# Kernel optimization log

Hardware: AMD Instinct MI355X
Metric: run time of the kernel (lower is better)

Reference implementation:

```python
import jax, jax.numpy as jnp
import numpy as np

B, T_ENC, T_DEC = 32, 512, 512
N_MELS, PRENET, ENC_H, ATTN_H, DEC_H, ATTN_D, N_FILT, KSIZE = 80, 256, 512, 1024, 1024, 128, 32, 31


def _lstm_cell(x, h, c, wih, whh, bih, bhh):
    gates = x @ wih.T + h @ whh.T + bih + bhh  # (B, 4H)
    i, f, g, o = jnp.split(gates, 4, axis=-1)  # torch LSTMCell gate order
    c2 = jax.nn.sigmoid(f) * c + jax.nn.sigmoid(i) * jnp.tanh(g)
    h2 = jax.nn.sigmoid(o) * jnp.tanh(c2)
    return h2, c2


def setup_inputs() -> dict:
    key = jax.random.key(0)
    ks = jax.random.split(key, 24)
    s = lambda k, shape, scale: jax.random.normal(k, shape, dtype=jnp.float32) * scale
    inp = {
        'encoder_output': s(ks[0], (B, T_ENC, ENC_H), 1.0),
        'targets': s(ks[1], (B, T_DEC, N_MELS), 1.0),
        'prenet_w1': s(ks[2], (PRENET, N_MELS), 0.05),
        'prenet_b1': jnp.zeros((PRENET,), jnp.float32),
        'prenet_w2': s(ks[3], (PRENET, PRENET), 0.05),
        'prenet_b2': jnp.zeros((PRENET,), jnp.float32),
        'M_w': s(ks[4], (ATTN_D, ENC_H), 0.04),
        'Q_w': s(ks[5], (ATTN_D, ATTN_H), 0.03),
        'W_w': s(ks[6], (1, ATTN_D), 0.08),
        'L_w': s(ks[7], (ATTN_D, N_FILT), 0.1),
        'conv_w': s(ks[8], (N_FILT, 2, KSIZE), 0.1),
        'attn_wih': s(ks[9], (4 * ATTN_H, ENC_H + PRENET), 0.02),
        'attn_whh': s(ks[10], (4 * ATTN_H, ATTN_H), 0.02),
        'attn_bih': jnp.zeros((4 * ATTN_H,), jnp.float32),
        'attn_bhh': jnp.zeros((4 * ATTN_H,), jnp.float32),
        'dec_wih': s(ks[11], (4 * DEC_H, ATTN_H + ENC_H), 0.02),
        'dec_whh': s(ks[12], (4 * DEC_H, DEC_H), 0.02),
        'dec_bih': jnp.zeros((4 * DEC_H,), jnp.float32),
        'dec_bhh': jnp.zeros((4 * DEC_H,), jnp.float32),
        'proj_w': s(ks[13], (N_MELS, DEC_H + ENC_H), 0.02),
        'proj_b': jnp.zeros((N_MELS,), jnp.float32),
    }
    return inp


def _decoder(encoder_output, targets, prenet_w1, prenet_b1, prenet_w2, prenet_b2,
             M_w, Q_w, W_w, L_w, conv_w,
             attn_wih, attn_whh, attn_bih, attn_bhh,
             dec_wih, dec_whh, dec_bih, dec_bhh, proj_w, proj_b):
    b, t_enc, _ = encoder_output.shape
    t_dec = targets.shape[1]
    pad = (KSIZE - 1) // 2

    # prenet over [zeros ; targets][:, :t_dec]  (eval mode: dropout off)
    dec_in = jnp.concatenate([jnp.zeros((b, 1, N_MELS), targets.dtype), targets], axis=1)[:, :t_dec]
    h = jax.nn.relu(dec_in @ prenet_w1.T + prenet_b1)
    prenet_out = jax.nn.relu(h @ prenet_w2.T + prenet_b2)  # (B, T_dec, prenet)

    processed_enc = encoder_output @ M_w.T  # (B, T_enc, attn_dim)

    def step(carry, x):
        ah, ac, dh, dc, aw, aws, ctx = carry
        # attention LSTM
        cell_in = jnp.concatenate([x, ctx], axis=-1)
        ah, ac = _lstm_cell(cell_in, ah, ac, attn_wih, attn_whh, attn_bih, attn_bhh)
        # location-sensitive attention
        prev_attn = jnp.stack([aw, aws], axis=1)  # (B, 2, T_enc)
        pa = jax.lax.conv_general_dilated(prev_attn, conv_w, (1,), [(pad, pad)],
                                          dimension_numbers=('NCH', 'OIH', 'NCH'))  # (B, F, T)
        pa = jnp.einsum('bft,df->btd', pa, L_w)  # (B, T, attn_dim)
        q = (ah @ Q_w.T)[:, None, :]  # (B, 1, attn_dim)
        energies = jnp.tanh(q + processed_enc + pa) @ W_w[0]  # (B, T)
        aw = jax.nn.softmax(energies, axis=1)
        ctx = jnp.einsum('bt,bte->be', aw, encoder_output)
        aws = aws + aw
        # decoder LSTM
        dcell_in = jnp.concatenate([ah, ctx], axis=-1)
        dh, dc = _lstm_cell(dcell_in, dh, dc, dec_wih, dec_whh, dec_bih, dec_bhh)
        out = jnp.concatenate([dh, ctx], axis=-1) @ proj_w.T + proj_b  # (B, n_mels)
        return (ah, ac, dh, dc, aw, aws, ctx), (out, aw)

    z = lambda d: jnp.zeros((b, d), encoder_output.dtype)
    carry0 = (z(ATTN_H), z(ATTN_H), z(DEC_H), z(DEC_H), z(t_enc), z(t_enc), z(ENC_H))
    xs = jnp.swapaxes(prenet_out, 0, 1)  # (T_dec, B, prenet)
    _, (mels, aligns) = jax.lax.scan(step, carry0, xs)
    mel_outputs = jnp.swapaxes(mels, 0, 1)      # (B, T_dec, n_mels)
    alignments = jnp.swapaxes(aligns, 0, 1)     # (B, T_dec, T_enc)
    return mel_outputs, alignments


def reference(encoder_output, targets, prenet_w1, prenet_b1, prenet_w2, prenet_b2,
              M_w, Q_w, W_w, L_w, conv_w,
              attn_wih, attn_whh, attn_bih, attn_bhh,
              dec_wih, dec_whh, dec_bih, dec_bhh, proj_w, proj_b):
    return _decoder(encoder_output, targets, prenet_w1, prenet_b1, prenet_w2, prenet_b2,
                    M_w, Q_w, W_w, L_w, conv_w,
                    attn_wih, attn_whh, attn_bih, attn_bhh,
                    dec_wih, dec_whh, dec_bih, dec_bhh, proj_w, proj_b)
```

## Files before the change

### kernel.cpp

```cpp
#include <hip/hip_runtime.h>
#include <hip/hip_fp16.h>
#include <cstddef>

typedef unsigned int uint32;

#define B_   32
#define TE_  512
#define TD_  512
#define NM_  80
#define PRE_ 256
#define EH_  512
#define AH_  1024
#define AD_  128

__device__ __forceinline__ float sigf(float x) { return 1.0f / (1.0f + expf(-x)); }

__device__ __forceinline__ float agl(const float* p) {
  return __hip_atomic_load(p, __ATOMIC_RELAXED, __HIP_MEMORY_SCOPE_AGENT);
}
__device__ __forceinline__ void ags(float* p, float v) {
  __hip_atomic_store(p, v, __ATOMIC_RELAXED, __HIP_MEMORY_SCOPE_AGENT);
}

__device__ __forceinline__ void gsync(uint32* bar, unsigned bep) {
  __syncthreads();
  if (threadIdx.x == 0) {
    asm volatile("s_waitcnt vmcnt(0)" ::: "memory");
    uint32* leaf = bar + (blockIdx.x >> 5) * 32;
    uint32* root = bar + 256;
    uint32 prev = __hip_atomic_fetch_add(leaf, 1u, __ATOMIC_RELAXED, __HIP_MEMORY_SCOPE_AGENT);
    if (prev + 1u == 32u * bep)
      __hip_atomic_fetch_add(root, 1u, __ATOMIC_RELAXED, __HIP_MEMORY_SCOPE_AGENT);
    int spins = 0;
    while (__hip_atomic_load(root, __ATOMIC_RELAXED, __HIP_MEMORY_SCOPE_AGENT) < 8u * bep) {
      __builtin_amdgcn_s_sleep(2);
      if (++spins > 20000000) break;
    }
  }
  __syncthreads();
}

__device__ __forceinline__ float rowsum16(float v) {
  int vi;
  vi = __float_as_int(v);
  v += __int_as_float(__builtin_amdgcn_update_dpp(0, vi, 0xB1, 0xF, 0xF, true));
  vi = __float_as_int(v);
  v += __int_as_float(__builtin_amdgcn_update_dpp(0, vi, 0x4E, 0xF, 0xF, true));
  vi = __float_as_int(v);
  v += __int_as_float(__builtin_amdgcn_update_dpp(0, vi, 0x124, 0xF, 0xF, true));
  vi = __float_as_int(v);
  v += __int_as_float(__builtin_amdgcn_update_dpp(0, vi, 0x128, 0xF, 0xF, true));
  return v;
}

__global__ __launch_bounds__(256) void k_pack_lstm2(
    const float* __restrict__ awih, const float* __restrict__ awhh,
    const float* __restrict__ dwih, const float* __restrict__ dwhh,
    uint32* __restrict__ wal, uint32* __restrict__ wdl, uint32* __restrict__ wdt)
{
  long gid = blockIdx.x * 256L + threadIdx.x;
  const long N1 = 3686400L, N2 = 4603904L, N3 = 655360L;
  if (gid < N1) {
    int blk = (int)(gid / 28800), rem = (int)(gid % 28800);
    int r2 = rem % 900;
    int ks = rem / 900;
    uint32 out = 0;
    if (r2 < 896) {
      int kq = r2 >> 4, rd = r2 & 15;
      int k = kq * 32 + ks;
      int rp0 = blk * 32 + 2 * rd, rp1 = rp0 + 1;
      int row0 = (rp0 & 3) * 1024 + (rp0 >> 2);
      int row1 = (rp1 & 3) * 1024 + (rp1 >> 2);
      float w0 = (k < 768) ? awih[(size_t)row0 * 768 + k] : awhh[(size_t)row0 * 1024 + k - 768];
      float w1 = (k < 768) ? awih[(size_t)row1 * 768 + k] : awhh[(size_t)row1 * 1024 + k - 768];
      __half2 h = __floats2half2_rn(w0, w1);
      out = *(uint32*)&h;
    }
    wal[gid] = out;
  } else if (gid < N1 + N2) {
    long g = gid - N1;
    int blk = (int)(g / 35968), rem = (int)(g % 35968);
    int r2 = rem % 1124;
    int ks = rem / 1124;
    uint32 out = 0;
    if (r2 < 1120) {
      int kq = r2 >> 4, rd = r2 & 15;
      int k = kq * 32 + ks;
      int rp0 = blk * 32 + 2 * rd, rp1 = rp0 + 1;
      int row0 = (rp0 & 3) * 1024 + (rp0 >> 2);
      int row1 = (rp1 & 3) * 1024 + (rp1 >> 2);
      float w0 = (k < 1536) ? dwih[(size_t)row0 * 1536 + k] : dwhh[(size_t)row0 * 1024 + k - 1536];
      float w1 = (k < 1536) ? dwih[(size_t)row1 * 1536 + k] : dwhh[(size_t)row1 * 1024 + k - 1536];
      __half2 h = __floats2half2_rn(w0, w1);
      out = *(uint32*)&h;
    }
    wdl[g] = out;
  } else if (gid < N1 + N2 + N3) {
    long g = gid - N1 - N2;
    int blk = (int)(g / 5120), rem = (int)(g % 5120);
    int rd2 = rem & 3, rg = (rem >> 2) & 3, ks = (rem >> 4) & 31, i = rem >> 9;
    int k = 2240 + 32 * i + ks;
    int r0 = rg * 8 + 2 * rd2;
    int rp0 = blk * 32 + r0, rp1 = rp0 + 1;
    int row0 = (rp0 & 3) * 1024 + (rp0 >> 2);
    int row1 = (rp1 & 3) * 1024 + (rp1 >> 2);
    float w0 = (k < 1536) ? dwih[(size_t)row0 * 1536 + k] : dwhh[(size_t)row0 * 1024 + k - 1536];
    float w1 = (k < 1536) ? dwih[(size_t)row1 * 1536 + k] : dwhh[(size_t)row1 * 1024 + k - 1536];
    __half2 h = __floats2half2_rn(w0, w1);
    wdt[g] = *(uint32*)&h;
  }
}

__global__ __launch_bounds__(256) void k_pack_small(
    const float* __restrict__ w1, const float* __restrict__ w2,
    const float* __restrict__ mw, const float* __restrict__ pw,
    const float* __restrict__ abih, const float* __restrict__ abhh,
    const float* __restrict__ dbih, const float* __restrict__ dbhh,
    const float* __restrict__ lw, const float* __restrict__ cw,
    float* __restrict__ w1t, float* __restrict__ w2t, float* __restrict__ mt,
    float* __restrict__ pjt, float* __restrict__ ba, float* __restrict__ bd,
    float* __restrict__ lc)
{
  int gid = blockIdx.x * 256 + threadIdx.x;
  if (gid < 20480) { int k = gid / 256, j = gid % 256; w1t[gid] = w1[j * 80 + k]; return; }
  gid -= 20480;
  if (gid < 65536) { int k = gid / 256, j = gid % 256; w2t[gid] = w2[j * 256 + k]; return; }
  gid -= 65536;
  if (gid < 65536) { int e = gid / 128, d = gid % 128; mt[gid] = mw[d * 512 + e]; return; }
  gid -= 65536;
  if (gid < 122880) { int k = gid / 80, m = gid % 80; pjt[gid] = pw[m * 1536 + k]; return; }
  gid -= 122880;
  if (gid < 4096) { int j = gid >> 2, g = gid & 3, row = g * 1024 + j; ba[gid] = abih[row] + abhh[row]; return; }
  gid -= 4096;
  if (gid < 4096) { int j = gid >> 2, g = gid & 3, row = g * 1024 + j; bd[gid] = dbih[row] + dbhh[row]; return; }
  gid -= 4096;
  if (gid < 7936) {
    int c = gid / (31 * 128), rem = gid % (31 * 128);
    int kk = rem / 128, d = rem % 128;
    float s = 0.f;
    for (int f = 0; f < 32; ++f) s += lw[d * 32 + f] * cw[(f * 2 + c) * 31 + kk];
    lc[gid] = s;
  }
}

__global__ __launch_bounds__(256) void k_prenet(
    const float* __restrict__ targets, const float* __restrict__ w1t,
    const float* __restrict__ b1, const float* __restrict__ w2t,
    const float* __restrict__ b2, float* __restrict__ pn)
{
  int t = blockIdx.x, tid = threadIdx.x;
  __shared__ float X[32][80];
  __shared__ float h1[256][33];
  for (int i = tid; i < 2560; i += 256) {
    int b = i / 80, m = i % 80;
    X[b][m] = (t == 0) ? 0.f : targets[((size_t)b * TD_ + (t - 1)) * NM_ + m];
  }
  __syncthreads();
  int j = tid;
  float bj = b1[j];
  for (int bt = 0; bt < 4; ++bt) {
    float acc[8];
#pragma unroll
    for (int i = 0; i < 8; ++i) acc[i] = bj;
    for (int k = 0; k < 80; ++k) {
      float w = w1t[k * 256 + j];
#pragma unroll
      for (int i = 0; i < 8; ++i) acc[i] += w * X[bt * 8 + i][k];
    }
#pragma unroll
    for (int i = 0; i < 8; ++i) h1[j][bt * 8 + i] = fmaxf(acc[i], 0.f);
  }
  __syncthreads();
  float cj = b2[j];
  float* out = pn + (size_t)t * PRE_ * B_;
  for (int bt = 0; bt < 4; ++bt) {
    float acc[8];
#pragma unroll
    for (int i = 0; i < 8; ++i) acc[i] = cj;
    for (int k = 0; k < 256; ++k) {
      float w = w2t[k * 256 + j];
#pragma unroll
      for (int i = 0; i < 8; ++i) acc[i] += w * h1[k][bt * 8 + i];
    }
#pragma unroll
    for (int i = 0; i < 8; ++i) out[j * 32 + bt * 8 + i] = fmaxf(acc[i], 0.f);
  }
}

__global__ __launch_bounds__(256) void k_penc(
    const float* __restrict__ enc, const float* __restrict__ mt,
    float* __restrict__ penc)
{
  int t = blockIdx.x, tid = threadIdx.x;
  __shared__ float encL[32][256];
  __shared__ float red[128][8][2];
  int d = tid & 127, s = tid >> 7;
  float acc[4][8];
#pragma unroll
  for (int bt = 0; bt < 4; ++bt)
#pragma unroll
    for (int i = 0; i < 8; ++i) acc[bt][i] = 0.f;
  for (int eh = 0; eh < 2; ++eh) {
    for (int i = tid; i < 8192; i += 256) {
      int b = i >> 8, e = i & 255;
      encL[b][e] = enc[((size_t)b * TE_ + t) * EH_ + eh * 256 + e];
    }
    __syncthreads();
    for (int bt = 0; bt < 4; ++bt) {
      for (int el = s * 128; el < s * 128 + 128; ++el) {
        float w = mt[(eh * 256 + el) * 128 + d];
#pragma unroll
        for (int i = 0; i < 8; ++i) acc[bt][i] += w * encL[bt * 8 + i][el];
      }
    }
    __syncthreads();
  }
  for (int bt = 0; bt < 4; ++bt) {
#pragma unroll
    for (int i = 0; i < 8; ++i) red[d][i][s] = acc[bt][i];
    __syncthreads();
    if (s == 0) {
#pragma unroll
      for (int i = 0; i < 8; ++i)
        penc[((size_t)t * AD_ + d) * 32 + bt * 8 + i] = red[d][i][0] + red[d][i][1];
    }
    __syncthreads();
  }
}

__global__ __launch_bounds__(256) void k_enct(
    const float* __restrict__ enc, __half* __restrict__ enct)
{
  int blk = blockIdx.x, tid = threadIdx.x;
  int b = blk >> 6, t0 = ((blk >> 3) & 7) * 64, e0 = (blk & 7) * 64;
  __shared__ float tile[64][65];
  for (int i = 0; i < 16; ++i) {
    int tl = i * 4 + (tid >> 6), e = tid & 63;
    tile[tl][e] = enc[((size_t)b * TE_ + t0 + tl) * EH_ + e0 + e];
  }
  __syncthreads();
  for (int i = 0; i < 16; ++i) {
    int el = i * 4 + (tid >> 6), tl = tid & 63;
    enct[((size_t)b * EH_ + e0 + el) * TE_ + t0 + tl] = __float2half(tile[tl][el]);
  }
}

struct KP {
  const uint32* wal; const uint32* wdl; const uint4* wdt;
  const float* pn; const float* penc; const __half* enct;
  const float* qw; const float* ww; const float* pjt; const float* pjb;
  const float* lc; const float* ba; const float* bd;
  float* ahv; float* ac; float* dhv; float* dc; float* ctxv;
  float* awv; float* awsv;
  float* enp; float* mel; float* align;
  uint32* bar; int pv;
};

__device__ __forceinline__ void fma2(uint4 wv, const float* __restrict__ XC,
                                     int xb, float* acc)
{
  const __half2* hp = (const __half2*)&wv;
  float w[8];
#pragma unroll
  for (int d = 0; d < 4; ++d) {
    float2 f = __half22float2(hp[d]);
    w[2 * d] = f.x; w[2 * d + 1] = f.y;
  }
  float4 xa = *(const float4*)&XC[xb];
  float4 xc2 = *(const float4*)&XC[xb + 4];
  float x[8] = {xa.x, xa.y, xa.z, xa.w, xc2.x, xc2.y, xc2.z, xc2.w};
#pragma unroll
  for (int ri = 0; ri < 8; ++ri)
#pragma unroll
    for (int bi = 0; bi < 8; ++bi)
      acc[ri * 8 + bi] = fmaf(w[ri], x[bi], acc[ri * 8 + bi]);
}

__device__ __forceinline__ void lstm_finish(
    float* acc, float* __restrict__ GT, const float* __restrict__ bias,
    float* __restrict__ cst, float* __restrict__ hout,
    int rp0, int tid, int ks, int bq, int rg)
{
#pragma unroll
  for (int i = 0; i < 64; ++i) {
    float v = rowsum16(acc[i]);
    acc[i] = v + __shfl_xor(v, 16);
  }
  if (ks == 0) {
#pragma unroll
    for (int ri = 0; ri < 8; ++ri) {
      *(float4*)&GT[(rg * 8 + ri) * 32 + bq * 8] =
          make_float4(acc[ri * 8 + 0], acc[ri * 8 + 1], acc[ri * 8 + 2], acc[ri * 8 + 3]);
      *(float4*)&GT[(rg * 8 + ri) * 32 + bq * 8 + 4] =
          make_float4(acc[ri * 8 + 4], acc[ri * 8 + 5], acc[ri * 8 + 6], acc[ri * 8 + 7]);
    }
  }
  __syncthreads();
  if (tid < 256) {
    int jl = tid >> 5, b = tid & 31;
    float gi = GT[(jl * 4 + 0) * 32 + b] + bias[rp0 + jl * 4 + 0];
    float gf = GT[(jl * 4 + 1) * 32 + b] + bias[rp0 + jl * 4 + 1];
    float gg = GT[(jl * 4 + 2) * 32 + b] + bias[rp0 + jl * 4 + 2];
    float go = GT[(jl * 4 + 3) * 32 + b] + bias[rp0 + jl * 4 + 3];
    int j = (rp0 >> 2) + jl;
    float c0 = cst[j * 32 + b];
    float c2 = sigf(gf) * c0 + sigf(gi) * tanhf(gg);
    float h2 = sigf(go) * tanhf(c2);
    cst[j * 32 + b] = c2;
    ags(&hout[j * 32 + b], h2);
  }
}

__device__ __forceinline__ void run_lstm_a(const KP& p, int t,
    const float* __restrict__ ah_in, const float* __restrict__ ctx_in,
    float* __restrict__ ah_out,
    uint32* WlU, float* XC, float* GT, int tid, int ks, int bq, int rg,
    int kidx, int b4, int blk)
{
  float acc[64];
#pragma unroll
  for (int i = 0; i < 64; ++i) acc[i] = 0.f;
  const float* xp0 = p.pn + (size_t)t * 8192;
  const int wb = ks * 900 + rg * 4;
  const int xr = ks * 36 + bq * 8;
  auto srcA = [&](int kg) -> const float* {
    return (kg < 256) ? xp0 + (size_t)kg * 32
         : (kg < 768) ? ctx_in + (size_t)(kg - 256) * 32
                      : ah_in + (size_t)(kg - 768) * 32;
  };
  float4 st0 = *(const float4*)(srcA(kidx) + b4);
  float4 st1 = *(const float4*)(srcA(64 + kidx) + b4);
  for (int cb = 0; cb < 28; cb += 2) {
    __syncthreads();
    *(float4*)&XC[kidx * 36 + b4] = st0;
    __syncthreads();
    if (cb + 2 < 28) st0 = *(const float4*)(srcA((cb + 2) * 64 + kidx) + b4);
    fma2(*(const uint4*)&WlU[wb + (2 * cb) * 16], XC, xr, acc);
    fma2(*(const uint4*)&WlU[wb + (2 * cb + 1) * 16], XC, xr + 32 * 36, acc);
    __syncthreads();
    *(float4*)&XC[kidx * 36 + b4] = st1;
    __syncthreads();
    if (cb + 3 < 28) st1 = *(const float4*)(srcA((cb + 3) * 64 + kidx) + b4);
    fma2(*(const uint4*)&WlU[wb + (2 * cb + 2) * 16], XC, xr, acc);
    fma2(*(const uint4*)&WlU[wb + (2 * cb + 3) * 16], XC, xr + 32 * 36, acc);
  }
  lstm_finish(acc, GT, p.ba, p.ac, ah_out, blk * 32, tid, ks, bq, rg);
}

__device__ __forceinline__ void run_lstm_d(const KP& p,
    const float* __restrict__ xp0, const float* __restrict__ xp1,
    const float* __restrict__ xp2, float* __restrict__ dh_w,
    uint32* WlU, float* XC, float* GT,
    int tid, int ks, int bq, int rg, int kidx, int b4, int blk)
{
  float acc[64];
#pragma unroll
  for (int i = 0; i < 64; ++i) acc[i] = 0.f;
  const int wb = ks * 1124 + rg * 4;
  const int xr = ks * 36 + bq * 8;
  auto srcD = [&](int kg) -> const float* {
    return (kg < 1024) ? xp0 + (size_t)kg * 32
         : (kg < 1536) ? xp1 + (size_t)(kg - 1024) * 32
                       : xp2 + (size_t)(kg - 1536) * 32;
  };
  float4 st0 = *(const float4*)(srcD(kidx) + b4);
  float4 st1 = *(const float4*)(srcD(64 + kidx) + b4);
  for (int cb = 0; cb < 32; cb += 2) {
    __syncthreads();
    *(float4*)&XC[kidx * 36 + b4] = st0;
    __syncthreads();
    st0 = *(const float4*)(srcD((cb + 2) * 64 + kidx) + b4);
    fma2(*(const uint4*)&WlU[wb + (2 * cb) * 16], XC, xr, acc);
    fma2(*(const uint4*)&WlU[wb + (2 * cb + 1) * 16], XC, xr + 32 * 36, acc);
    __syncthreads();
    *(float4*)&XC[kidx * 36 + b4] = st1;
    __syncthreads();
    st1 = *(const float4*)(srcD((cb + 3) * 64 + kidx) + b4);
    fma2(*(const uint4*)&WlU[wb + (2 * cb + 2) * 16], XC, xr, acc);
    fma2(*(const uint4*)&WlU[wb + (2 * cb + 3) * 16], XC, xr + 32 * 36, acc);
  }
  const uint4* wg = p.wdt + (size_t)(blk - 128) * 1280;
  const int wi = ks * 4 + rg;
  uint4 twA0, twB0, twA1, twB1;
  __syncthreads(); *(float4*)&XC[kidx * 36 + b4] = st0; __syncthreads();
  st0 = *(const float4*)(srcD(34 * 64 + kidx) + b4);
  twA0 = wg[0 * 128 + wi]; twB0 = wg[1 * 128 + wi];
  fma2(*(const uint4*)&WlU[wb + 64 * 16], XC, xr, acc);
  fma2(*(const uint4*)&WlU[wb + 65 * 16], XC, xr + 32 * 36, acc);
  __syncthreads(); *(float4*)&XC[kidx * 36 + b4] = st1; __syncthreads();
  st1 = *(const float4*)(srcD(35 * 64 + kidx) + b4);
  twA1 = wg[2 * 128 + wi]; twB1 = wg[3 * 128 + wi];
  fma2(*(const uint4*)&WlU[wb + 66 * 16], XC, xr, acc);
  fma2(*(const uint4*)&WlU[wb + 67 * 16], XC, xr + 32 * 36, acc);
  __syncthreads(); *(float4*)&XC[kidx * 36 + b4] = st0; __syncthreads();
  st0 = *(const float4*)(srcD(36 * 64 + kidx) + b4);
  fma2(*(const uint4*)&WlU[wb + 68 * 16], XC, xr, acc);
  fma2(*(const uint4*)&WlU[wb + 69 * 16], XC, xr + 32 * 36, acc);
  __syncthreads(); *(float4*)&XC[kidx * 36 + b4] = st1; __syncthreads();
  st1 = *(const float4*)(srcD(37 * 64 + kidx) + b4);
  fma2(twA0, XC, xr, acc); fma2(twB0, XC, xr + 32 * 36, acc);
  twA0 = wg[4 * 128 + wi]; twB0 = wg[5 * 128 + wi];
  __syncthreads(); *(float4*)&XC[kidx * 36 + b4] = st0; __syncthreads();
  st0 = *(const float4*)(srcD(38 * 64 + kidx) + b4);
  fma2(twA1, XC, xr, acc); fma2(twB1, XC, xr + 32 * 36, acc);
  twA1 = wg[6 * 128 + wi]; twB1 = wg[7 * 128 + wi];
  __syncthreads(); *(float4*)&XC[kidx * 36 + b4] = st1; __syncthreads();
  st1 = *(const float4*)(srcD(39 * 64 + kidx) + b4);
  fma2(twA0, XC, xr, acc); fma2(twB0, XC, xr + 32 * 36, acc);
  twA0 = wg[8 * 128 + wi]; twB0 = wg[9 * 128 + wi];
  __syncthreads(); *(float4*)&XC[kidx * 36 + b4] = st0; __syncthreads();
  fma2(twA1, XC, xr, acc); fma2(twB1, XC, xr + 32 * 36, acc);
  __syncthreads(); *(float4*)&XC[kidx * 36 + b4] = st1; __syncthreads();
  fma2(twA0, XC, xr, acc); fma2(twB0, XC, xr + 32 * 36, acc);
  lstm_finish(acc, GT, p.bd, p.dc, dh_w, (blk - 128) * 32, tid, ks, bq, rg);
}

__device__ __forceinline__ void mel_block(
    const float* __restrict__ dhp, const float* __restrict__ ctp,
    const float* __restrict__ pjt, const float* __restrict__ pjb,
    float* __restrict__ mel, int bb, int tt, float* S, int tid)
{
  float* xo = S + 1536;
  float* ro = S + 3072;
  for (int i = tid; i < 1536; i += 512)
    xo[i] = (i < 1024) ? dhp[i * 32 + bb] : ctp[(i - 1024) * 32 + bb];
  __syncthreads();
  if (tid < 480) {
    int m = tid % 80, k2 = tid / 80;
    float a2 = 0.f;
    for (int k = k2 * 256; k < k2 * 256 + 256; ++k) a2 += pjt[k * 80 + m] * xo[k];
    ro[m * 8 + k2] = a2;
  }
  __syncthreads();
  if (tid < 80) {
    float s3 = pjb[tid];
#pragma unroll
    for (int k = 0; k < 6; ++k) s3 += ro[tid * 8 + k];
    mel[((size_t)bb * TD_ + tt) * NM_ + tid] = s3;
  }
}

__global__ __launch_bounds__(512) void k_step(KP p)
{
  extern __shared__ float LDSF[];
  const int blk = blockIdx.x, tid = threadIdx.x;
  const int ks = tid & 31, bq = (tid >> 5) & 3, rg = tid >> 7;
  const int kidx = tid >> 3, b4 = (tid & 7) * 4;
  const bool isA = blk < 128;
  float* SC = LDSF + (isA ? 28800 : 35968);
  float* XC = SC;
  float* GT = SC + 2304;
  uint32* WlU = (uint32*)LDSF;
  unsigned bep = 0;

  {
    const uint32* src = isA ? p.wal + (size_t)blk * 28800
                            : p.wdl + (size_t)(blk - 128) * 35968;
    int n4 = isA ? 7200 : 8992;
    for (int i = tid; i < n4; i += 512)
      ((uint4*)WlU)[i] = ((const uint4*)src)[i];
  }
  __syncthreads();

  for (int t = 0; t < TD_; ++t) {
    const int vc = t % p.pv;
    const int vn = (t + 1) % p.pv;
    const int vp = (t > 0) ? (t - 1) % p.pv : 0;
    const float* ah_in  = p.ahv + (size_t)vc * 32768;
    float*       ah_out = p.ahv + (size_t)vn * 32768;
    const float* ctx_in = p.ctxv + (size_t)vc * 16384;
    float*       ctx_out= p.ctxv + (size_t)vn * 16384;

    if (isA) {
      run_lstm_a(p, t, ah_in, ctx_in, ah_out, WlU, XC, GT, tid, ks, bq, rg, kidx, b4, blk);
    } else if (t > 0) {
      run_lstm_d(p, ah_in, ctx_in,
                 p.dhv + (size_t)vp * 32768, p.dhv + (size_t)vc * 32768,
                 WlU, XC, GT, tid, ks, bq, rg, kidx, b4, blk);
    }
    bep += 1; gsync(p.bar, bep);
    {
      int tc = blk >> 3, ds = blk & 7;
      int t0 = tc * 16, d0 = ds * 16;
      float* qs  = SC;
      float* wws = SC + 512;
      float* AHC = SC + 528;
      float* win = SC + 528;
      float* lcs = SC + 528 + 2944;

      const float* awsrc  = p.awv  + (size_t)vc * 16384;
      const float* awssrc = p.awsv + (size_t)vc * 16384;
      float winr[6];
#pragma unroll
      for (int k = 0; k < 6; ++k) {
        int i = tid + k * 512;
        float v = 0.f;
        if (i < 2944) {
          int c = i / 1472, r = (i >> 5) % 46, bbw = i & 31;
          int tg = t0 - 15 + r;
          if (tg >= 0 && tg < 512) v = (c ? awssrc : awsrc)[tg * 32 + bbw];
        }
        winr[k] = v;
      }
      float lcr[2];
#pragma unroll
      for (int k = 0; k < 2; ++k) {
        int i = tid + k * 512;
        lcr[k] = 0.f;
        if (i < 992) {
          int c = i / 496, kk = (i >> 4) % 31, dl2 = i & 15;
          lcr[k] = p.lc[(c * 31 + kk) * 128 + d0 + dl2];
        }
      }
      const int bbE = tid & 31, thE = tid >> 5;
      const int ttE = t0 + thE;
      float pencr[16];
#pragma unroll
      for (int dl2 = 0; dl2 < 16; ++dl2)
        pencr[dl2] = p.penc[((size_t)ttE * 128 + d0 + dl2) * 32 + bbE];
      float wwr = (tid < 16) ? p.ww[d0 + tid] : 0.f;

      int bb2 = tid & 31, dl = tid >> 5;
      const float* ahsrc = p.ahv + (size_t)vn * 32768;
      const float* qbase = p.qw + (size_t)(d0 + dl) * 1024;
      float qacc = 0.f;
      float4 sq0 = *(const float4*)(ahsrc + 0 * 2048 + tid * 4);
      float4 sq1 = *(const float4*)(ahsrc + 1 * 2048 + tid * 4);
      for (int cb = 0; cb < 16; cb += 2) {
        __syncthreads();
        *(float4*)(AHC + tid * 4) = sq0;
        __syncthreads();
        if (cb + 2 < 16) sq0 = *(const float4*)(ahsrc + (cb + 2) * 2048 + tid * 4);
        {
          const float* qrow = qbase + cb * 64;
#pragma unroll
          for (int jj = 0; jj < 64; jj += 4) {
            float4 qv = *(const float4*)(qrow + jj);
            qacc = fmaf(qv.x, AHC[(jj + 0) * 32 + bb2], qacc);
            qacc = fmaf(qv.y, AHC[(jj + 1) * 32 + bb2], qacc);
            qacc = fmaf(qv.z, AHC[(jj + 2) * 32 + bb2], qacc);
            qacc = fmaf(qv.w, AHC[(jj + 3) * 32 + bb2], qacc);
          }
        }
        __syncthreads();
        *(float4*)(AHC + tid * 4) = sq1;
        __syncthreads();
        if (cb + 3 < 16) sq1 = *(const float4*)(ahsrc + (cb + 3) * 2048 + tid * 4);
        {
          const float* qrow = qbase + (cb + 1) * 64;
#pragma unroll
          for (int jj = 0; jj < 64; jj += 4) {
            float4 qv = *(const float4*)(qrow + jj);
            qacc = fmaf(qv.x, AHC[(jj + 0) * 32 + bb2], qacc);
            qacc = fmaf(qv.y, AHC[(jj + 1) * 32 + bb2], qacc);
            qacc = fmaf(qv.z, AHC[(jj + 2) * 32 + bb2], qacc);
            qacc = fmaf(qv.w, AHC[(jj + 3) * 32 + bb2], qacc);
          }
        }
      }
      __syncthreads();
      qs[dl * 32 + bb2] = qacc;
      if (tid < 16) wws[tid] = wwr;
#pragma unroll
      for (int k = 0; k < 6; ++k) { int i = tid + k * 512; if (i < 2944) win[i] = winr[k]; }
#pragma unroll
      for (int k = 0; k < 2; ++k) { int i = tid + k * 512; if (i < 992) lcs[i] = lcr[k]; }
      __syncthreads();
      {
        float pa[16];
#pragma unroll
        for (int i = 0; i < 16; ++i) pa[i] = 0.f;
        for (int c = 0; c < 2; ++c) {
          for (int kk = 0; kk < 31; ++kk) {
            float wv = win[c * 1472 + (thE + kk) * 32 + bbE];
            const float4* lr = (const float4*)(lcs + c * 496 + kk * 16);
            float4 l0 = lr[0], l1 = lr[1], l2 = lr[2], l3 = lr[3];
            pa[0]  += l0.x * wv; pa[1]  += l0.y * wv; pa[2]  += l0.z * wv; pa[3]  += l0.w * wv;
            pa[4]  += l1.x * wv; pa[5]  += l1.y * wv; pa[6]  += l1.z * wv; pa[7]  += l1.w * wv;
            pa[8]  += l2.x * wv; pa[9]  += l2.y * wv; pa[10] += l2.z * wv; pa[11] += l2.w * wv;
            pa[12] += l3.x * wv; pa[13] += l3.y * wv; pa[14] += l3.z * wv; pa[15] += l3.w * wv;
          }
        }
        float epv = 0.f;
#pragma unroll
        for (int dl2 = 0; dl2 < 16; ++dl2) {
          float v = qs[dl2 * 32 + bbE] + pencr[dl2] + pa[dl2];
          epv += wws[dl2] * tanhf(v);
        }
        ags(&p.enp[(size_t)bbE * 4096 + ttE * 8 + ds], epv);
      }
    }
    bep += 1; gsync(p.bar, bep);
    {
      int bb = blk >> 3, et = blk & 7;
      float* awL = SC + 512;
      float* cr  = SC + 1024;
      int el = tid & 63, ts = tid >> 6;
      const uint32* eb = (const uint32*)(p.enct +
          ((size_t)(bb * 512 + et * 64 + el)) * 512 + ts * 64);
      uint32 ebr[32];
#pragma unroll
      for (int i = 0; i < 32; ++i) ebr[i] = eb[i];
      const float* epb = p.enp + (size_t)bb * 4096 + tid * 8;
      float e = agl(epb) + agl(epb + 1) + agl(epb + 2) + agl(epb + 3)
              + agl(epb + 4) + agl(epb + 5) + agl(epb + 6) + agl(epb + 7);
      float m = e;
#pragma unroll
      for (int k = 1; k < 64; k <<= 1) m = fmaxf(m, __shfl_xor(m, k));
      int wv = tid >> 6;
      if ((tid & 63) == 0) SC[wv] = m;
      __syncthreads();
      m = SC[0];
#pragma unroll
      for (int k = 1; k < 8; ++k) m = fmaxf(m, SC[k]);
      float x = expf(e - m);
      float s = x;
#pragma unroll
      for (int k = 1; k < 64; k <<= 1) s += __shfl_xor(s, k);
      if ((tid & 63) == 0) SC[8 + wv] = s;
      __syncthreads();
      s = SC[8];
#pragma unroll
      for (int k = 1; k < 8; ++k) s += SC[8 + k];
      float a = x * (1.f / s);
      awL[tid] = a;
      __syncthreads();
      float acc = 0.f;
#pragma unroll
      for (int i = 0; i < 32; ++i) {
        float2 f = __half22float2(*(const __half2*)&ebr[i]);
        acc += awL[ts * 64 + 2 * i] * f.x + awL[ts * 64 + 2 * i + 1] * f.y;
      }
      cr[ts * 64 + el] = acc;
      __syncthreads();
      if (tid < 64) {
        float s2 = 0.f;
#pragma unroll
        for (int k = 0; k < 8; ++k) s2 += cr[k * 64 + tid];
        ags(&ctx_out[(et * 64 + tid) * 32 + bb], s2);
      }
      if (et == 0) {
        float osv = p.awsv[(size_t)vc * 16384 + tid * 32 + bb];
        ags(&p.awv[(size_t)vn * 16384 + tid * 32 + bb], a);
        ags(&p.awsv[(size_t)vn * 16384 + tid * 32 + bb], osv + a);
        p.align[((size_t)bb * TD_ + t) * TE_ + tid] = a;
      }
      if (et == 1 && t > 0) {
        mel_block(p.dhv + (size_t)vc * 32768, p.ctxv + (size_t)vc * 16384,
                  p.pjt, p.pjb, p.mel, bb, t - 1, SC, tid);
      }
    }
    bep += 1; gsync(p.bar, bep);
  }
  {
    const int v511 = 511 % p.pv, v512 = 512 % p.pv;
    if (!isA) {
      run_lstm_d(p, p.ahv + (size_t)v512 * 32768, p.ctxv + (size_t)v512 * 16384,
                 p.dhv + (size_t)v511 * 32768, p.dhv + (size_t)v512 * 32768,
                 WlU, XC, GT, tid, ks, bq, rg, kidx, b4, blk);
    }
    bep += 1; gsync(p.bar, bep);
    if (blk < 32) {
      mel_block(p.dhv + (size_t)v512 * 32768, p.ctxv + (size_t)v512 * 16384,
                p.pjt, p.pjb, p.mel, blk, 511, SC, tid);
    }
  }
}

extern "C" void kernel_launch(void* const* d_in, const int* in_sizes, int n_in,
                              void* d_out, int out_size, void* d_ws, size_t ws_size,
                              hipStream_t stream)
{
  const float* enc     = (const float*)d_in[0];
  const float* targets = (const float*)d_in[1];
  const float* pw1  = (const float*)d_in[2];
  const float* pb1  = (const float*)d_in[3];
  const float* pw2  = (const float*)d_in[4];
  const float* pb2  = (const float*)d_in[5];
  const float* mw   = (const float*)d_in[6];
  const float* qw   = (const float*)d_in[7];
  const float* www  = (const float*)d_in[8];
  const float* lw   = (const float*)d_in[9];
  const float* cw   = (const float*)d_in[10];
  const float* awih = (const float*)d_in[11];
  const float* awhh = (const float*)d_in[12];
  const float* abih = (const float*)d_in[13];
  const float* abhh = (const float*)d_in[14];
  const float* dwih = (const float*)d_in[15];
  const float* dwhh = (const float*)d_in[16];
  const float* dbih = (const float*)d_in[17];
  const float* dbhh = (const float*)d_in[18];
  const float* pjw  = (const float*)d_in[19];
  const float* pjb  = (const float*)d_in[20];

  uint32* wsb = (uint32*)d_ws;
  size_t o = 0;
  auto F = [&](size_t n) { size_t r = o; o += n; return r; };
  size_t oWAL = F(3686400), oWDL = F(4603904), oWDT = F(655360);
  size_t oENCT = F(4194304);
  size_t oPN = F(4194304), oPENC = F(2097152);
  size_t oW1T = F(20480), oW2T = F(65536), oMT = F(65536), oPJT = F(122880);
  size_t oLC = F(7936), oBA = F(4096), oBD = F(4096);
  size_t oZR = o;
  size_t oAC = F(32768), oDC = F(32768), oBAR = F(1024);
  size_t zr_dw = o - oZR;
  o = (o + 31) & ~(size_t)31;
  size_t fixed_dw = o;
  size_t avail_dw = ws_size / 4;
  long pvl = (avail_dw > fixed_dw) ? (long)((avail_dw - fixed_dw) / 114688) : 0;
  int pv = (pvl < 3) ? 3 : (pvl > 513 ? 513 : (int)pvl);
  size_t oAHV  = F((size_t)pv * 32768);
  size_t oDHV  = F((size_t)pv * 32768);
  size_t oCTXV = F((size_t)pv * 16384);
  size_t oAWV  = F((size_t)pv * 16384);
  size_t oAWSV = F((size_t)pv * 16384);
  size_t oENP  = oW1T;

  hipMemsetAsync(wsb + oZR, 0, zr_dw * 4, stream);
  hipMemsetAsync(wsb + oAHV, 0, (size_t)32768 * 4, stream);
  hipMemsetAsync(wsb + oDHV, 0, (size_t)32768 * 4, stream);
  hipMemsetAsync(wsb + oCTXV, 0, (size_t)16384 * 4, stream);
  hipMemsetAsync(wsb + oAWV, 0, (size_t)16384 * 4, stream);
  hipMemsetAsync(wsb + oAWSV, 0, (size_t)16384 * 4, stream);

  float* mel = (float*)d_out;
  float* align = mel + (size_t)B_ * TD_ * NM_;

  k_pack_lstm2<<<34944, 256, 0, stream>>>(awih, awhh, dwih, dwhh,
                                          wsb + oWAL, wsb + oWDL, wsb + oWDT);
  k_pack_small<<<1135, 256, 0, stream>>>(pw1, pw2, mw, pjw, abih, abhh, dbih, dbhh,
                                         lw, cw,
                                         (float*)(wsb + oW1T), (float*)(wsb + oW2T),
                                         (float*)(wsb + oMT), (float*)(wsb + oPJT),
                                         (float*)(wsb + oBA), (float*)(wsb + oBD),
                                         (float*)(wsb + oLC));
  k_prenet<<<512, 256, 0, stream>>>(targets, (float*)(wsb + oW1T), pb1,
                                    (float*)(wsb + oW2T), pb2, (float*)(wsb + oPN));
  k_penc<<<512, 256, 0, stream>>>(enc, (float*)(wsb + oMT), (float*)(wsb + oPENC));
  k_enct<<<2048, 256, 0, stream>>>(enc, (__half*)(wsb + oENCT));

  KP kp;
  kp.wal = wsb + oWAL; kp.wdl = wsb + oWDL; kp.wdt = (const uint4*)(wsb + oWDT);
  kp.pn = (float*)(wsb + oPN); kp.penc = (float*)(wsb + oPENC);
  kp.enct = (__half*)(wsb + oENCT);
  kp.qw = qw; kp.ww = www; kp.pjt = (float*)(wsb + oPJT); kp.pjb = pjb;
  kp.lc = (float*)(wsb + oLC); kp.ba = (float*)(wsb + oBA); kp.bd = (float*)(wsb + oBD);
  kp.ahv = (float*)(wsb + oAHV); kp.ac = (float*)(wsb + oAC);
  kp.dhv = (float*)(wsb + oDHV); kp.dc = (float*)(wsb + oDC);
  kp.ctxv = (float*)(wsb + oCTXV);
  kp.awv = (float*)(wsb + oAWV); kp.awsv = (float*)(wsb + oAWSV);
  kp.enp = (float*)(wsb + oENP); kp.mel = mel; kp.align = align;
  kp.bar = wsb + oBAR; kp.pv = pv;

  hipFuncSetAttribute((const void*)k_step,
                      hipFuncAttributeMaxDynamicSharedMemorySize, 161728);
  void* kargs[] = { &kp };
  hipLaunchCooperativeKernel((const void*)k_step, dim3(256), dim3(512), kargs,
                             161728, stream);
}
```

Baseline: 97.26 ms.

## Deepen global-load prefetch to four stages and hoist encoder loads across barrier

The staging loops in both LSTM phases and the query projection now keep four register-held float4 prefetches in flight instead of two, so each global load has more time to land before its slice is written to shared memory. The per-block encoder-slice loads used in the context computation are moved ahead of the grid barrier into the attention-energy phase, overlapping their latency with earlier work. A waves-per-EU attribute pins occupancy at two waves. The cost is higher register pressure from the extra prefetch registers and the 32 encoder registers now live across the barrier, which could cause spills.

```diff
diff --git a/kernel.cpp b/kernel.cpp
--- a/kernel.cpp
+++ b/kernel.cpp
@@ -330,19 +330,25 @@
   };
   float4 st0 = *(const float4*)(srcA(kidx) + b4);
   float4 st1 = *(const float4*)(srcA(64 + kidx) + b4);
-  for (int cb = 0; cb < 28; cb += 2) {
-    __syncthreads();
-    *(float4*)&XC[kidx * 36 + b4] = st0;
-    __syncthreads();
-    if (cb + 2 < 28) st0 = *(const float4*)(srcA((cb + 2) * 64 + kidx) + b4);
+  float4 st2 = *(const float4*)(srcA(128 + kidx) + b4);
+  float4 st3 = *(const float4*)(srcA(192 + kidx) + b4);
+  for (int cb = 0; cb < 28; cb += 4) {
+    __syncthreads(); *(float4*)&XC[kidx * 36 + b4] = st0; __syncthreads();
+    if (cb + 4 < 28) st0 = *(const float4*)(srcA((cb + 4) * 64 + kidx) + b4);
     fma2(*(const uint4*)&WlU[wb + (2 * cb) * 16], XC, xr, acc);
     fma2(*(const uint4*)&WlU[wb + (2 * cb + 1) * 16], XC, xr + 32 * 36, acc);
-    __syncthreads();
-    *(float4*)&XC[kidx * 36 + b4] = st1;
-    __syncthreads();
-    if (cb + 3 < 28) st1 = *(const float4*)(srcA((cb + 3) * 64 + kidx) + b4);
+    __syncthreads(); *(float4*)&XC[kidx * 36 + b4] = st1; __syncthreads();
+    if (cb + 5 < 28) st1 = *(const float4*)(srcA((cb + 5) * 64 + kidx) + b4);
     fma2(*(const uint4*)&WlU[wb + (2 * cb + 2) * 16], XC, xr, acc);
     fma2(*(const uint4*)&WlU[wb + (2 * cb + 3) * 16], XC, xr + 32 * 36, acc);
+    __syncthreads(); *(float4*)&XC[kidx * 36 + b4] = st2; __syncthreads();
+    if (cb + 6 < 28) st2 = *(const float4*)(srcA((cb + 6) * 64 + kidx) + b4);
+    fma2(*(const uint4*)&WlU[wb + (2 * cb + 4) * 16], XC, xr, acc);
+    fma2(*(const uint4*)&WlU[wb + (2 * cb + 5) * 16], XC, xr + 32 * 36, acc);
+    __syncthreads(); *(float4*)&XC[kidx * 36 + b4] = st3; __syncthreads();
+    if (cb + 7 < 28) st3 = *(const float4*)(srcA((cb + 7) * 64 + kidx) + b4);
+    fma2(*(const uint4*)&WlU[wb + (2 * cb + 6) * 16], XC, xr, acc);
+    fma2(*(const uint4*)&WlU[wb + (2 * cb + 7) * 16], XC, xr + 32 * 36, acc);
   }
   lstm_finish(acc, GT, p.ba, p.ac, ah_out, blk * 32, tid, ks, bq, rg);
 }
@@ -365,52 +371,56 @@
   };
   float4 st0 = *(const float4*)(srcD(kidx) + b4);
   float4 st1 = *(const float4*)(srcD(64 + kidx) + b4);
-  for (int cb = 0; cb < 32; cb += 2) {
-    __syncthreads();
-    *(float4*)&XC[kidx * 36 + b4] = st0;
-    __syncthreads();
-    st0 = *(const float4*)(srcD((cb + 2) * 64 + kidx) + b4);
+  float4 st2 = *(const float4*)(srcD(128 + kidx) + b4);
+  float4 st3 = *(const float4*)(srcD(192 + kidx) + b4);
+  for (int cb = 0; cb < 32; cb += 4) {
+    __syncthreads(); *(float4*)&XC[kidx * 36 + b4] = st0; __syncthreads();
+    st0 = *(const float4*)(srcD((cb + 4) * 64 + kidx) + b4);
     fma2(*(const uint4*)&WlU[wb + (2 * cb) * 16], XC, xr, acc);
     fma2(*(const uint4*)&WlU[wb + (2 * cb + 1) * 16], XC, xr + 32 * 36, acc);
-    __syncthreads();
-    *(float4*)&XC[kidx * 36 + b4] = st1;
-    __syncthreads();
-    st1 = *(const float4*)(srcD((cb + 3) * 64 + kidx) + b4);
+    __syncthreads(); *(float4*)&XC[kidx * 36 + b4] = st1; __syncthreads();
+    st1 = *(const float4*)(srcD((cb + 5) * 64 + kidx) + b4);
     fma2(*(const uint4*)&WlU[wb + (2 * cb + 2) * 16], XC, xr, acc);
     fma2(*(const uint4*)&WlU[wb + (2 * cb + 3) * 16], XC, xr + 32 * 36, acc);
+    __syncthreads(); *(float4*)&XC[kidx * 36 + b4] = st2; __syncthreads();
+    st2 = *(const float4*)(srcD((cb + 6) * 64 + kidx) + b4);
+    fma2(*(const uint4*)&WlU[wb + (2 * cb + 4) * 16], XC, xr, acc);
+    fma2(*(const uint4*)&WlU[wb + (2 * cb + 5) * 16], XC, xr + 32 * 36, acc);
+    __syncthreads(); *(float4*)&XC[kidx * 36 + b4] = st3; __syncthreads();
+    st3 = *(const float4*)(srcD((cb + 7) * 64 + kidx) + b4);
+    fma2(*(const uint4*)&WlU[wb + (2 * cb + 6) * 16], XC, xr, acc);
+    fma2(*(const uint4*)&WlU[wb + (2 * cb + 7) * 16], XC, xr + 32 * 36, acc);
   }
   const uint4* wg = p.wdt + (size_t)(blk - 128) * 1280;
   const int wi = ks * 4 + rg;
   uint4 twA0, twB0, twA1, twB1;
   __syncthreads(); *(float4*)&XC[kidx * 36 + b4] = st0; __syncthreads();
-  st0 = *(const float4*)(srcD(34 * 64 + kidx) + b4);
+  st0 = *(const float4*)(srcD(36 * 64 + kidx) + b4);
   twA0 = wg[0 * 128 + wi]; twB0 = wg[1 * 128 + wi];
   fma2(*(const uint4*)&WlU[wb + 64 * 16], XC, xr, acc);
   fma2(*(const uint4*)&WlU[wb + 65 * 16], XC, xr + 32 * 36, acc);
   __syncthreads(); *(float4*)&XC[kidx * 36 + b4] = st1; __syncthreads();
-  st1 = *(const float4*)(srcD(35 * 64 + kidx) + b4);
+  st1 = *(const float4*)(srcD(37 * 64 + kidx) + b4);
   twA1 = wg[2 * 128 + wi]; twB1 = wg[3 * 128 + wi];
   fma2(*(const uint4*)&WlU[wb + 66 * 16], XC, xr, acc);
   fma2(*(const uint4*)&WlU[wb + 67 * 16], XC, xr + 32 * 36, acc);
-  __syncthreads(); *(float4*)&XC[kidx * 36 + b4] = st0; __syncthreads();
-  st0 = *(const float4*)(srcD(36 * 64 + kidx) + b4);
+  __syncthreads(); *(float4*)&XC[kidx * 36 + b4] = st2; __syncthreads();
+  st2 = *(const float4*)(srcD(38 * 64 + kidx) + b4);
   fma2(*(const uint4*)&WlU[wb + 68 * 16], XC, xr, acc);
   fma2(*(const uint4*)&WlU[wb + 69 * 16], XC, xr + 32 * 36, acc);
-  __syncthreads(); *(float4*)&XC[kidx * 36 + b4] = st1; __syncthreads();
-  st1 = *(const float4*)(srcD(37 * 64 + kidx) + b4);
+  __syncthreads(); *(float4*)&XC[kidx * 36 + b4] = st3; __syncthreads();
+  st3 = *(const float4*)(srcD(39 * 64 + kidx) + b4);
   fma2(twA0, XC, xr, acc); fma2(twB0, XC, xr + 32 * 36, acc);
   twA0 = wg[4 * 128 + wi]; twB0 = wg[5 * 128 + wi];
   __syncthreads(); *(float4*)&XC[kidx * 36 + b4] = st0; __syncthreads();
-  st0 = *(const float4*)(srcD(38 * 64 + kidx) + b4);
   fma2(twA1, XC, xr, acc); fma2(twB1, XC, xr + 32 * 36, acc);
   twA1 = wg[6 * 128 + wi]; twB1 = wg[7 * 128 + wi];
   __syncthreads(); *(float4*)&XC[kidx * 36 + b4] = st1; __syncthreads();
-  st1 = *(const float4*)(srcD(39 * 64 + kidx) + b4);
   fma2(twA0, XC, xr, acc); fma2(twB0, XC, xr + 32 * 36, acc);
   twA0 = wg[8 * 128 + wi]; twB0 = wg[9 * 128 + wi];
-  __syncthreads(); *(float4*)&XC[kidx * 36 + b4] = st0; __syncthreads();
+  __syncthreads(); *(float4*)&XC[kidx * 36 + b4] = st2; __syncthreads();
   fma2(twA1, XC, xr, acc); fma2(twB1, XC, xr + 32 * 36, acc);
-  __syncthreads(); *(float4*)&XC[kidx * 36 + b4] = st1; __syncthreads();
+  __syncthreads(); *(float4*)&XC[kidx * 36 + b4] = st3; __syncthreads();
   fma2(twA0, XC, xr, acc); fma2(twB0, XC, xr + 32 * 36, acc);
   lstm_finish(acc, GT, p.bd, p.dc, dh_w, (blk - 128) * 32, tid, ks, bq, rg);
 }
@@ -440,7 +450,8 @@
   }
 }
 
-__global__ __launch_bounds__(512) void k_step(KP p)
+__global__ __attribute__((amdgpu_waves_per_eu(2, 2))) __launch_bounds__(512)
+void k_step(KP p)
 {
   extern __shared__ float LDSF[];
   const int blk = blockIdx.x, tid = threadIdx.x;
@@ -470,6 +481,7 @@
     float*       ah_out = p.ahv + (size_t)vn * 32768;
     const float* ctx_in = p.ctxv + (size_t)vc * 16384;
     float*       ctx_out= p.ctxv + (size_t)vn * 16384;
+    uint32 ebr[32];
 
     if (isA) {
       run_lstm_a(p, t, ah_in, ctx_in, ah_out, WlU, XC, GT, tid, ks, bq, rg, kidx, b4, blk);
@@ -488,6 +500,13 @@
       float* win = SC + 528;
       float* lcs = SC + 528 + 2944;
 
+      {
+        int elP = tid & 63, tsP = tid >> 6;
+        const uint32* ebp = (const uint32*)(p.enct +
+            ((size_t)((blk >> 3) * 512 + (blk & 7) * 64 + elP)) * 512 + tsP * 64);
+#pragma unroll
+        for (int i = 0; i < 32; ++i) ebr[i] = ebp[i];
+      }
       const float* awsrc  = p.awv  + (size_t)vc * 16384;
       const float* awssrc = p.awsv + (size_t)vc * 16384;
       float winr[6];
@@ -526,28 +545,19 @@
       float qacc = 0.f;
       float4 sq0 = *(const float4*)(ahsrc + 0 * 2048 + tid * 4);
       float4 sq1 = *(const float4*)(ahsrc + 1 * 2048 + tid * 4);
-      for (int cb = 0; cb < 16; cb += 2) {
-        __syncthreads();
-        *(float4*)(AHC + tid * 4) = sq0;
-        __syncthreads();
-        if (cb + 2 < 16) sq0 = *(const float4*)(ahsrc + (cb + 2) * 2048 + tid * 4);
-        {
-          const float* qrow = qbase + cb * 64;
-#pragma unroll
-          for (int jj = 0; jj < 64; jj += 4) {
-            float4 qv = *(const float4*)(qrow + jj);
-            qacc = fmaf(qv.x, AHC[(jj + 0) * 32 + bb2], qacc);
-            qacc = fmaf(qv.y, AHC[(jj + 1) * 32 + bb2], qacc);
-            qacc = fmaf(qv.z, AHC[(jj + 2) * 32 + bb2], qacc);
-            qacc = fmaf(qv.w, AHC[(jj + 3) * 32 + bb2], qacc);
+      float4 sq2 = *(const float4*)(ahsrc + 2 * 2048 + tid * 4);
+      float4 sq3 = *(const float4*)(ahsrc + 3 * 2048 + tid * 4);
+      for (int cb = 0; cb < 16; cb += 4) {
+#pragma unroll
+        for (int u = 0; u < 4; ++u) {
+          __syncthreads();
+          *(float4*)(AHC + tid * 4) = (u == 0) ? sq0 : (u == 1) ? sq1 : (u == 2) ? sq2 : sq3;
+          __syncthreads();
+          if (cb + u + 4 < 16) {
+            float4 nv = *(const float4*)(ahsrc + (cb + u + 4) * 2048 + tid * 4);
+            if (u == 0) sq0 = nv; else if (u == 1) sq1 = nv; else if (u == 2) sq2 = nv; else sq3 = nv;
           }
-        }
-        __syncthreads();
-        *(float4*)(AHC + tid * 4) = sq1;
-        __syncthreads();
-        if (cb + 3 < 16) sq1 = *(const float4*)(ahsrc + (cb + 3) * 2048 + tid * 4);
-        {
-          const float* qrow = qbase + (cb + 1) * 64;
+          const float* qrow = qbase + (cb + u) * 64;
 #pragma unroll
           for (int jj = 0; jj < 64; jj += 4) {
             float4 qv = *(const float4*)(qrow + jj);
@@ -596,11 +606,6 @@
       float* awL = SC + 512;
       float* cr  = SC + 1024;
       int el = tid & 63, ts = tid >> 6;
-      const uint32* eb = (const uint32*)(p.enct +
-          ((size_t)(bb * 512 + et * 64 + el)) * 512 + ts * 64);
-      uint32 ebr[32];
-#pragma unroll
-      for (int i = 0; i < 32; ++i) ebr[i] = eb[i];
       const float* epb = p.enp + (size_t)bb * 4096 + tid * 8;
       float e = agl(epb) + agl(epb + 1) + agl(epb + 2) + agl(epb + 3)
               + agl(epb + 4) + agl(epb + 5) + agl(epb + 6) + agl(epb + 7);
```

Result: slower. 173.2 ms (+78.1%).
